# Kernel optimization log

Hardware: AMD Instinct MI355X
Metric: run time of the kernel (lower is better)

Reference implementation:

```python
import jax, jax.numpy as jnp
import numpy as np

D_MODEL = 1024
NHEAD = 16


def unitnorm(v):
    # F.normalize(v, dim=-1): v / max(||v||_2, 1e-12)
    n = jnp.sqrt(jnp.sum(v * v, axis=-1, keepdims=True))
    return v / jnp.maximum(n, 1e-12)


def setup_inputs() -> dict:
    key = jax.random.key(0)
    ks = jax.random.split(key, 14)
    d = D_MODEL
    sc = 1.0 / np.sqrt(d)
    inp = jax.random.normal(ks[0], (2048, 8, d), dtype=jnp.float32)
    def lin(kw, kb, out_dim):
        W = jax.random.uniform(kw, (out_dim, d), minval=-sc, maxval=sc, dtype=jnp.float32)
        b = jax.random.uniform(kb, (out_dim,), minval=-sc, maxval=sc, dtype=jnp.float32)
        return W, b
    Wq_w, Wq_b = lin(ks[1], ks[2], d)
    Wk_w, Wk_b = lin(ks[3], ks[4], d)
    Wv_w, Wv_b = lin(ks[5], ks[6], d)
    Wo_w, Wo_b = lin(ks[7], ks[8], d)
    Ww_w, Ww_b = lin(ks[9], ks[10], NHEAD)
    Wr_w, Wr_b = lin(ks[11], ks[12], NHEAD)
    return {"inp": inp, "Wq_w": Wq_w, "Wq_b": Wq_b, "Wk_w": Wk_w, "Wk_b": Wk_b,
            "Wv_w": Wv_w, "Wv_b": Wv_b, "Wo_w": Wo_w, "Wo_b": Wo_b,
            "Ww_w": Ww_w, "Ww_b": Ww_b, "Wr_w": Wr_w, "Wr_b": Wr_b}


def reference(inp, Wq_w, Wq_b, Wk_w, Wk_b, Wv_w, Wv_b, Wo_w, Wo_b, Ww_w, Ww_b, Wr_w, Wr_b):
    src = inp  # src=None path
    S, B, d = inp.shape
    n = NHEAD
    # torch Linear: x @ W.T + b
    k = (src @ Wk_w.T + Wk_b).reshape(S, B, n, -1)
    v = (src @ Wv_w.T + Wv_b).reshape(S, B, n, -1)
    q = (inp @ Wq_w.T + Wq_b).reshape(S, B, n, -1)
    k = unitnorm(k)
    q = unitnorm(q)
    w = jax.nn.sigmoid(src @ Ww_w.T + Ww_b)            # [S,B,n]
    A = jnp.einsum('sbnq,sbnv->bnvq', k, v * w[:, :, :, None])
    r = jax.nn.sigmoid(inp @ Wr_w.T + Wr_b)            # [S,B,n]
    out = jnp.einsum('sbnq,bnvq->sbnv', q, A) * r[:, :, :, None]
    out = out.reshape(S, B, d)
    out = out @ Wo_w.T + Wo_b
    return (out, A)
```

## Files before the change

### kernel.cpp

```cpp
#include <hip/hip_runtime.h>
#include <cstdint>
#include <cstddef>


typedef __bf16 bf16x8 __attribute__((ext_vector_type(8)));
typedef float  f32x4  __attribute__((ext_vector_type(4)));
typedef unsigned short u16x8 __attribute__((ext_vector_type(8)));
typedef unsigned short u16x4 __attribute__((ext_vector_type(4)));

#define ROWS 16384
#define DM   1024

__device__ __forceinline__ unsigned short f2bf(float f) {
  unsigned int u = __builtin_bit_cast(unsigned int, f);
  u += 0x7FFFu + ((u >> 16) & 1u);
  return (unsigned short)(u >> 16);
}
__device__ __forceinline__ float bf2f(unsigned short h) {
  unsigned int u = ((unsigned int)h) << 16;
  return __builtin_bit_cast(float, u);
}
__device__ __forceinline__ float sigm(float x) { return 1.0f / (1.0f + __expf(-x)); }

__device__ __forceinline__ void gload_lds16(const void* g, void* l) {
  __builtin_amdgcn_global_load_lds((__attribute__((address_space(1))) void*)(g),
                                   (__attribute__((address_space(3))) void*)(l),
                                   16, 0, 0);
}

__global__ __launch_bounds__(256) void k_cast_x(const float* __restrict__ X,
                                                unsigned short* __restrict__ Xb) {
  size_t i = ((size_t)blockIdx.x * 256 + threadIdx.x) * 8;
  f32x4 a = *(const f32x4*)(X + i);
  f32x4 b = *(const f32x4*)(X + i + 4);
  u16x8 o;
  o[0] = f2bf(a[0]); o[1] = f2bf(a[1]); o[2] = f2bf(a[2]); o[3] = f2bf(a[3]);
  o[4] = f2bf(b[0]); o[5] = f2bf(b[1]); o[6] = f2bf(b[2]); o[7] = f2bf(b[3]);
  *(u16x8*)(Xb + i) = o;
}

__global__ __launch_bounds__(256) void k_pack_w(
    const float* __restrict__ Wq, const float* __restrict__ Wk, const float* __restrict__ Wv,
    const float* __restrict__ Wo, const float* __restrict__ Ww, const float* __restrict__ Wr,
    const float* __restrict__ bq, const float* __restrict__ bk, const float* __restrict__ bv,
    const float* __restrict__ bw, const float* __restrict__ br,
    unsigned short* __restrict__ Wpack, float* __restrict__ biasP,
    unsigned short* __restrict__ WRw, float* __restrict__ biasWR,
    unsigned short* __restrict__ Wob) {
  int r = blockIdx.x, t = threadIdx.x;
  const float* src; float bias = 0.0f; unsigned short* dst; float* bdst;
  if (r < 1024)      { src = Wq + (size_t)r * DM;          bias = bq[r];        dst = Wpack + (size_t)r * DM;          bdst = biasP + r; }
  else if (r < 2048) { src = Wk + (size_t)(r - 1024) * DM; bias = bk[r - 1024]; dst = Wpack + (size_t)r * DM;          bdst = biasP + r; }
  else if (r < 3072) { src = Wv + (size_t)(r - 2048) * DM; bias = bv[r - 2048]; dst = Wpack + (size_t)r * DM;          bdst = biasP + r; }
  else if (r < 3088) { src = Ww + (size_t)(r - 3072) * DM; bias = bw[r - 3072]; dst = WRw + (size_t)(r - 3072) * DM;   bdst = biasWR + (r - 3072); }
  else if (r < 3104) { src = Wr + (size_t)(r - 3088) * DM; bias = br[r - 3088]; dst = WRw + (size_t)(r - 3072) * DM;   bdst = biasWR + (r - 3072); }
  else               { src = Wo + (size_t)(r - 3104) * DM;                      dst = Wob + (size_t)(r - 3104) * DM;   bdst = nullptr; }
  int c = t * 4;
  f32x4 v = *(const f32x4*)(src + c);
  u16x4 o;
  o[0] = f2bf(v[0]); o[1] = f2bf(v[1]); o[2] = f2bf(v[2]); o[3] = f2bf(v[3]);
  *(u16x4*)(dst + c) = o;
  if (t == 0 && bdst) *bdst = bias;
}

__global__ __launch_bounds__(256) void k_wr(const unsigned short* __restrict__ Xb,
                                            const unsigned short* __restrict__ WRw,
                                            const float* __restrict__ biasWR,
                                            float* __restrict__ WRf) {
  __shared__ __bf16 sA[128 * 64];
  __shared__ __bf16 sB[32 * 64];
  int t = threadIdx.x, lane = t & 63, wid = t >> 6;
  int m0 = blockIdx.x * 128;
  int l15 = lane & 15, l4 = lane >> 4;
  f32x4 acc[2][2];
#pragma unroll
  for (int i = 0; i < 2; ++i)
#pragma unroll
    for (int j = 0; j < 2; ++j) acc[i][j] = (f32x4){0.f, 0.f, 0.f, 0.f};
  int srow = t >> 3, schunk = (t & 7) * 8;
  for (int kt = 0; kt < DM; kt += 64) {
#pragma unroll
    for (int c = 0; c < 4; ++c)
      gload_lds16(Xb + (size_t)(m0 + c * 32 + srow) * DM + kt + schunk,
                  (void*)(sA + c * 2048 + wid * 512));
    gload_lds16(WRw + (size_t)srow * DM + kt + schunk, (void*)(sB + wid * 512));
    __syncthreads();
#pragma unroll
    for (int ks = 0; ks < 2; ++ks) {
      bf16x8 fa[2], fb[2];
#pragma unroll
      for (int mi = 0; mi < 2; ++mi)
        fa[mi] = *(const bf16x8*)(sA + (wid * 32 + mi * 16 + l15) * 64 + (ks * 4 + l4) * 8);
#pragma unroll
      for (int ni = 0; ni < 2; ++ni)
        fb[ni] = *(const bf16x8*)(sB + (ni * 16 + l15) * 64 + (ks * 4 + l4) * 8);
#pragma unroll
      for (int mi = 0; mi < 2; ++mi)
#pragma unroll
        for (int ni = 0; ni < 2; ++ni)
          acc[mi][ni] = __builtin_amdgcn_mfma_f32_16x16x32_bf16(fa[mi], fb[ni], acc[mi][ni], 0, 0, 0);
    }
    __syncthreads();
  }
#pragma unroll
  for (int mi = 0; mi < 2; ++mi)
#pragma unroll
    for (int e = 0; e < 4; ++e) {
      int row = m0 + wid * 32 + mi * 16 + 4 * l4 + e;
#pragma unroll
      for (int ni = 0; ni < 2; ++ni)
        WRf[(size_t)row * 32 + ni * 16 + l15] = acc[mi][ni][e] + biasWR[ni * 16 + l15];
    }
}


#define VMW(N)  asm volatile("s_waitcnt vmcnt(" #N ")" ::: "memory")
#define LGKM(N) asm volatile("s_waitcnt lgkmcnt(" #N ")" ::: "memory")
#define SB0     __builtin_amdgcn_sched_barrier(0)

__device__ __forceinline__ void stageT(const unsigned short* __restrict__ Asrc,
                                       const unsigned short* __restrict__ Bsrc,
                                       int kt, __bf16* sm, int sb, int w) {
#pragma unroll
  for (int c = 0; c < 2; ++c)
    gload_lds16(Asrc + (size_t)c * 128 * DM + kt, (void*)(sm + sb + c * 4096 + w * 512));
#pragma unroll
  for (int c = 0; c < 2; ++c)
    gload_lds16(Bsrc + (size_t)c * 128 * DM + kt, (void*)(sm + sb + 8192 + c * 4096 + w * 512));
}

__device__ __forceinline__ void rdFA(bf16x8 (&fa)[8], const __bf16* base, const int (&aoff)[8]) {
#pragma unroll
  for (int mi = 0; mi < 8; ++mi) fa[mi] = *(const bf16x8*)(base + aoff[mi]);
}
__device__ __forceinline__ void rdFB(bf16x8 (&fb)[4], const __bf16* base, const int (&boff)[4]) {
#pragma unroll
  for (int ni = 0; ni < 4; ++ni) fb[ni] = *(const bf16x8*)(base + boff[ni]);
}

#define MFMA32(FB)                                                                   \
  do {                                                                               \
    __builtin_amdgcn_s_setprio(1);                                                   \
    _Pragma("unroll") for (int mi = 0; mi < 8; ++mi)                                 \
    _Pragma("unroll") for (int ni = 0; ni < 4; ++ni)                                 \
      acc[mi][ni] = __builtin_amdgcn_mfma_f32_16x16x32_bf16(fa[mi], FB[ni],          \
                                                            acc[mi][ni], 0, 0, 0);  \
    __builtin_amdgcn_s_setprio(0);                                                   \
    SB0;                                                                             \
  } while (0)

__device__ __forceinline__ void gemm_d4(const unsigned short* __restrict__ Ag,
                                        const unsigned short* __restrict__ Bg,
                                        __bf16* sm, f32x4 (&acc)[8][4],
                                        int m0, int n0, int lane, int w) {
  const int wm = w >> 2, wn = w & 3;
  const int l15 = lane & 15, l4 = lane >> 4;
  const int t = w * 64 + lane;
  const int srow = t >> 2;
  const int schunk = ((t & 3) ^ ((srow >> 1) & 3)) * 8;
  const unsigned short* Asrc = Ag + (size_t)(m0 + srow) * DM + schunk;
  const unsigned short* Bsrc = Bg + (size_t)(n0 + srow) * DM + schunk;

  int aoff[8], boff[4];
#pragma unroll
  for (int mi = 0; mi < 8; ++mi) {
    int r = wm * 128 + mi * 16 + l15;
    aoff[mi] = r * 32 + ((l4 ^ ((r >> 1) & 3)) << 3);
  }
#pragma unroll
  for (int ni = 0; ni < 4; ++ni) {
    int r = wn * 64 + ni * 16 + l15;
    boff[ni] = 8192 + r * 32 + ((l4 ^ ((r >> 1) & 3)) << 3);
  }

  bf16x8 fa[8], fbA[4], fbB[4];
  stageT(Asrc, Bsrc, 0,  sm, 0,     w);
  stageT(Asrc, Bsrc, 32, sm, 16384, w);
  stageT(Asrc, Bsrc, 64, sm, 32768, w);
  VMW(8);
  __builtin_amdgcn_s_barrier(); SB0;
  rdFB(fbA, sm, boff);
  rdFA(fa, sm, aoff);
  VMW(4);
  __builtin_amdgcn_s_barrier(); SB0;

  int sb = 49152;
  int rb = 16384;
  for (int i = 0; i < 14; ++i) {
    stageT(Asrc, Bsrc, (2 * i + 3) * 32, sm, sb, w); sb = (sb + 16384) & 65535;
    rdFB(fbB, sm + rb, boff);
    LGKM(4); SB0;
    MFMA32(fbA);
    rdFA(fa, sm + rb, aoff); rb = (rb + 16384) & 65535;
    VMW(4);
    __builtin_amdgcn_s_barrier(); SB0;
    stageT(Asrc, Bsrc, (2 * i + 4) * 32, sm, sb, w); sb = (sb + 16384) & 65535;
    rdFB(fbA, sm + rb, boff);
    LGKM(4); SB0;
    MFMA32(fbB);
    rdFA(fa, sm + rb, aoff); rb = (rb + 16384) & 65535;
    VMW(4);
    __builtin_amdgcn_s_barrier(); SB0;
  }
  stageT(Asrc, Bsrc, 992, sm, sb, w);
  rdFB(fbB, sm + rb, boff);
  LGKM(4); SB0;
  MFMA32(fbA);
  rdFA(fa, sm + rb, aoff); rb = (rb + 16384) & 65535;
  VMW(4);
  __builtin_amdgcn_s_barrier(); SB0;
  rdFB(fbA, sm + rb, boff);
  LGKM(4); SB0;
  MFMA32(fbB);
  rdFA(fa, sm + rb, aoff); rb = (rb + 16384) & 65535;
  VMW(0);
  __builtin_amdgcn_s_barrier(); SB0;
  rdFB(fbB, sm + rb, boff);
  LGKM(4); SB0;
  MFMA32(fbA);
  rdFA(fa, sm + rb, aoff);
  LGKM(0); SB0;
  MFMA32(fbB);
}

__global__ __launch_bounds__(512, 2) void k_gemm_qkv6(
    const unsigned short* __restrict__ Xb, const unsigned short* __restrict__ Wpack,
    const float* __restrict__ biasP, const float* __restrict__ WRf,
    unsigned short* __restrict__ Qb, unsigned short* __restrict__ Kb,
    unsigned short* __restrict__ Vb) {
  __shared__ __bf16 sm[65536];
  const int t = threadIdx.x, lane = t & 63, w = t >> 6;
  const int wm = w >> 2, wn = w & 3;
  const int l15 = lane & 15, l4 = lane >> 4;
  int orig = blockIdx.x;
  int wg = (orig & 7) * 96 + (orig >> 3);
  const int m0 = (wg & 63) << 8;
  const int n0 = (wg >> 6) << 8;
  f32x4 acc[8][4];
#pragma unroll
  for (int i = 0; i < 8; ++i)
#pragma unroll
    for (int j = 0; j < 4; ++j) acc[i][j] = (f32x4){0.f, 0.f, 0.f, 0.f};
  gemm_d4(Xb, Wpack, sm, acc, m0, n0, lane, w);

  const int colbase = n0 + wn * 64;
  float bb[4];
#pragma unroll
  for (int ni = 0; ni < 4; ++ni) bb[ni] = biasP[colbase + ni * 16 + l15];

  if (colbase < 2048) {
    unsigned short* dstp = (colbase < 1024) ? Qb : Kb;
    int coff = (colbase < 1024) ? colbase : (colbase - 1024);
#pragma unroll
    for (int mi = 0; mi < 8; ++mi)
#pragma unroll
      for (int e = 0; e < 4; ++e) {
        float v[4]; float ssq = 0.f;
#pragma unroll
        for (int ni = 0; ni < 4; ++ni) { v[ni] = acc[mi][ni][e] + bb[ni]; ssq += v[ni] * v[ni]; }
        ssq += __shfl_xor(ssq, 1);
        ssq += __shfl_xor(ssq, 2);
        ssq += __shfl_xor(ssq, 4);
        ssq += __shfl_xor(ssq, 8);
        float sc = 1.0f / fmaxf(sqrtf(ssq), 1e-12f);
        int row = m0 + wm * 128 + mi * 16 + 4 * l4 + e;
#pragma unroll
        for (int ni = 0; ni < 4; ++ni)
          dstp[(size_t)row * DM + coff + ni * 16 + l15] = f2bf(v[ni] * sc);
      }
  } else {
    int hv = (colbase - 2048) >> 6;
    int coff = colbase - 2048;
#pragma unroll
    for (int mi = 0; mi < 8; ++mi)
#pragma unroll
      for (int e = 0; e < 4; ++e) {
        int row = m0 + wm * 128 + mi * 16 + 4 * l4 + e;
        float wgt = sigm(WRf[(size_t)row * 32 + hv]);
#pragma unroll
        for (int ni = 0; ni < 4; ++ni)
          Vb[(size_t)row * DM + coff + ni * 16 + l15] = f2bf((acc[mi][ni][e] + bb[ni]) * wgt);
      }
  }
}

__global__ __launch_bounds__(512, 2) void k_gemm_out6(
    const unsigned short* __restrict__ Ob, const unsigned short* __restrict__ Wob,
    const float* __restrict__ bo, float* __restrict__ Out) {
  __shared__ __bf16 sm[65536];
  const int t = threadIdx.x, lane = t & 63, w = t >> 6;
  const int wm = w >> 2, wn = w & 3;
  const int l15 = lane & 15, l4 = lane >> 4;
  int orig = blockIdx.x;
  int wg = (orig & 7) * 32 + (orig >> 3);
  const int m0 = (wg & 63) << 8;
  const int n0 = (wg >> 6) << 8;
  f32x4 acc[8][4];
#pragma unroll
  for (int i = 0; i < 8; ++i)
#pragma unroll
    for (int j = 0; j < 4; ++j) acc[i][j] = (f32x4){0.f, 0.f, 0.f, 0.f};
  gemm_d4(Ob, Wob, sm, acc, m0, n0, lane, w);

  float bb[4];
#pragma unroll
  for (int ni = 0; ni < 4; ++ni) bb[ni] = bo[n0 + wn * 64 + ni * 16 + l15];
#pragma unroll
  for (int mi = 0; mi < 8; ++mi)
#pragma unroll
    for (int e = 0; e < 4; ++e) {
      int row = m0 + wm * 128 + mi * 16 + 4 * l4 + e;
#pragma unroll
      for (int ni = 0; ni < 4; ++ni) {
        int col = n0 + wn * 64 + ni * 16 + l15;
        Out[(size_t)row * DM + col] = acc[mi][ni][e] + bb[ni];
      }
    }
}

__global__ __launch_bounds__(256, 2) void k_gemm_A(const unsigned short* __restrict__ Kb,
                                                   const unsigned short* __restrict__ Vb,
                                                   float* __restrict__ Apart) {
  __shared__ __bf16 sK[64 * 64];
  __shared__ __bf16 sV[64 * 64];
  int t = threadIdx.x, lane = t & 63, wid = t >> 6;
  int bn = blockIdx.x & 127, sk = blockIdx.x >> 7;
  int b = bn >> 4, n = bn & 15;
  f32x4 acc[4];
#pragma unroll
  for (int j = 0; j < 4; j++) acc[j] = (f32x4){0.f, 0.f, 0.f, 0.f};
  int lrow = lane >> 3, lcol = (lane & 7) * 8;

  for (int st = sk * 1024; st < (sk + 1) * 1024; st += 64) {
#pragma unroll
    for (int c = 0; c < 2; c++) {
      int r0 = wid * 16 + c * 8;
      size_t g = ((size_t)(st + r0 + lrow) * 8 + b) * DM + n * 64 + lcol;
      gload_lds16(Kb + g, (void*)(sK + r0 * 64));
      gload_lds16(Vb + g, (void*)(sV + r0 * 64));
    }
    __syncthreads();
#pragma unroll
    for (int kk = 0; kk < 64; kk += 32) {
      bf16x8 av, bv[4];
#pragma unroll
      for (int e = 0; e < 8; e++)
        av[e] = sV[(kk + 8 * (lane >> 4) + e) * 64 + wid * 16 + (lane & 15)];
#pragma unroll
      for (int jn = 0; jn < 4; jn++)
#pragma unroll
        for (int e = 0; e < 8; e++)
          bv[jn][e] = sK[(kk + 8 * (lane >> 4) + e) * 64 + jn * 16 + (lane & 15)];
#pragma unroll
      for (int jn = 0; jn < 4; jn++)
        acc[jn] = __builtin_amdgcn_mfma_f32_16x16x32_bf16(av, bv[jn], acc[jn], 0, 0, 0);
    }
    __syncthreads();
  }
  float* Ap = Apart + (size_t)(sk * 128 + bn) * 4096;
#pragma unroll
  for (int jn = 0; jn < 4; jn++) {
#pragma unroll
    for (int e = 0; e < 4; e++) {
      int i = wid * 16 + 4 * (lane >> 4) + e;
      int j = jn * 16 + (lane & 15);
      Ap[i * 64 + j] = acc[jn][e];
    }
  }
}

__global__ __launch_bounds__(256) void k_reduceA(const float* __restrict__ Apart,
                                                 float* __restrict__ Aout,
                                                 unsigned short* __restrict__ Abf) {
  int bn = blockIdx.x, t = threadIdx.x;
  size_t base = (size_t)bn * 4096 + t * 16;
#pragma unroll
  for (int j = 0; j < 4; ++j) {
    f32x4 x = *(const f32x4*)(Apart + base + j * 4);
    f32x4 y = *(const f32x4*)(Apart + (size_t)128 * 4096 + base + j * 4);
    x += y;
    *(f32x4*)(Aout + base + j * 4) = x;
    u16x4 o;
    o[0] = f2bf(x[0]); o[1] = f2bf(x[1]); o[2] = f2bf(x[2]); o[3] = f2bf(x[3]);
    *(u16x4*)(Abf + base + j * 4) = o;
  }
}

__global__ __launch_bounds__(256, 2) void k_gemm_o2(const unsigned short* __restrict__ Qb,
                                                    const unsigned short* __restrict__ Abf,
                                                    const float* __restrict__ WRf,
                                                    unsigned short* __restrict__ Ob) {
  __shared__ __bf16 sQ[128 * 64];
  __shared__ __bf16 sA[64 * 64];
  int t = threadIdx.x, lane = t & 63, wid = t >> 6;
  int bn = blockIdx.x & 127, stile = blockIdx.x >> 7;
  int b = bn >> 4, n = bn & 15;
  int s0 = stile * 128;
  int lrow = lane >> 3, lcol = (lane & 7) * 8;
#pragma unroll
  for (int c = 0; c < 4; c++) {
    int r0 = wid * 32 + c * 8;
    gload_lds16(Qb + ((size_t)(s0 + r0 + lrow) * 8 + b) * DM + n * 64 + lcol,
                (void*)(sQ + r0 * 64));
  }
#pragma unroll
  for (int c = 0; c < 2; c++) {
    int r0 = wid * 16 + c * 8;
    gload_lds16(Abf + (size_t)bn * 4096 + (size_t)(r0 + lrow) * 64 + lcol,
                (void*)(sA + r0 * 64));
  }
  __syncthreads();
  f32x4 acc[2][4];
#pragma unroll
  for (int i = 0; i < 2; i++)
#pragma unroll
    for (int j = 0; j < 4; j++) acc[i][j] = (f32x4){0.f, 0.f, 0.f, 0.f};
#pragma unroll
  for (int kk = 0; kk < 64; kk += 32) {
    bf16x8 aq[2], bA[4];
#pragma unroll
    for (int mi = 0; mi < 2; mi++)
      aq[mi] = *(const bf16x8*)(sQ + (wid * 32 + mi * 16 + (lane & 15)) * 64 + kk + 8 * (lane >> 4));
#pragma unroll
    for (int ni = 0; ni < 4; ni++)
      bA[ni] = *(const bf16x8*)(sA + (ni * 16 + (lane & 15)) * 64 + kk + 8 * (lane >> 4));
#pragma unroll
    for (int mi = 0; mi < 2; mi++)
#pragma unroll
      for (int ni = 0; ni < 4; ni++)
        acc[mi][ni] = __builtin_amdgcn_mfma_f32_16x16x32_bf16(aq[mi], bA[ni], acc[mi][ni], 0, 0, 0);
  }
#pragma unroll
  for (int mi = 0; mi < 2; mi++) {
#pragma unroll
    for (int e = 0; e < 4; e++) {
      int srow = wid * 32 + mi * 16 + 4 * (lane >> 4) + e;
      size_t row = (size_t)(s0 + srow) * 8 + b;
      float rv = sigm(WRf[row * 32 + 16 + n]);
#pragma unroll
      for (int ni = 0; ni < 4; ni++)
        Ob[row * DM + n * 64 + ni * 16 + (lane & 15)] = f2bf(acc[mi][ni][e] * rv);
    }
  }
}

extern "C" void kernel_launch(void* const* d_in, const int* in_sizes, int n_in,
                              void* d_out, int out_size, void* d_ws, size_t ws_size,
                              hipStream_t stream) {
  (void)in_sizes; (void)n_in; (void)out_size; (void)ws_size;
  const float* X  = (const float*)d_in[0];
  const float* Wq = (const float*)d_in[1];  const float* bq = (const float*)d_in[2];
  const float* Wk = (const float*)d_in[3];  const float* bk = (const float*)d_in[4];
  const float* Wv = (const float*)d_in[5];  const float* bv = (const float*)d_in[6];
  const float* Wo = (const float*)d_in[7];  const float* bo = (const float*)d_in[8];
  const float* Ww = (const float*)d_in[9];  const float* bw = (const float*)d_in[10];
  const float* Wr = (const float*)d_in[11]; const float* br = (const float*)d_in[12];

  char* ws = (char*)d_ws;
  unsigned short* Wpack = (unsigned short*)(ws + 0);
  float*          Apart = (float*)(ws + 0);
  unsigned short* Abf   = (unsigned short*)(ws + 4194304);
  float*          biasP = (float*)(ws + 6291456);
  unsigned short* WRw   = (unsigned short*)(ws + 6303744);
  float*          biasWR= (float*)(ws + 6369280);
  unsigned short* Wob   = (unsigned short*)(ws + 6369408);
  unsigned short* Xb    = (unsigned short*)(ws + 8466560);
  unsigned short* Ob    = Xb;
  unsigned short* Qb    = (unsigned short*)(ws + 42020992);
  unsigned short* Kb    = (unsigned short*)(ws + 75575424);
  unsigned short* Vb    = (unsigned short*)(ws + 109129856);
  float*          WRf   = (float*)(ws + 142684288);

  float* Out0 = (float*)d_out;
  float* Aout = Out0 + (size_t)ROWS * DM;

  k_cast_x<<<dim3(8192), dim3(256), 0, stream>>>(X, Xb);
  k_pack_w<<<dim3(4128), dim3(256), 0, stream>>>(Wq, Wk, Wv, Wo, Ww, Wr,
                                                 bq, bk, bv, bw, br,
                                                 Wpack, biasP, WRw, biasWR, Wob);
  k_wr<<<dim3(128), dim3(256), 0, stream>>>(Xb, WRw, biasWR, WRf);
  k_gemm_qkv6<<<dim3(768), dim3(512), 0, stream>>>(Xb, Wpack, biasP, WRf, Qb, Kb, Vb);
  k_gemm_A<<<dim3(256), dim3(256), 0, stream>>>(Kb, Vb, Apart);
  k_reduceA<<<dim3(128), dim3(256), 0, stream>>>(Apart, Aout, Abf);
  k_gemm_o2<<<dim3(2048), dim3(256), 0, stream>>>(Qb, Abf, WRf, Ob);
  k_gemm_out6<<<dim3(256), dim3(512), 0, stream>>>(Ob, Wob, bo, Out0);
}
```

Baseline: 241.9 us.

## Replace QKV GEMM with 128x128-tile double-buffered kernel at higher occupancy

The fused QKV projection GEMM moves from a 256x256-tile, 512-thread, hand-pipelined kernel to a simpler 128x128-tile, 256-thread kernel with two LDS buffers and 3 blocks per CU, launched as 3072 blocks. The aim is more blocks per CU and a less rigid schedule to hide latency, and the normalize and sigmoid epilogues are kept the same. The cost is lower data reuse per tile, so global and LDS traffic rise, and the hand-tuned waitcnt/barrier pipelining is gone. The output GEMM is only renamed.

Measured after the change: 256.8 us. +6.2%, slower.

```diff
diff --git a/kernel.cpp b/kernel.cpp
--- a/kernel.cpp
+++ b/kernel.cpp
@@ -114,6 +114,121 @@
 }
 
 
+#define STAGE128(P, kt)                                                             \
+  do {                                                                              \
+    _Pragma("unroll") for (int c = 0; c < 2; ++c)                                   \
+      gload_lds16(Asrc + (size_t)(c * 64) * DM + (kt),                              \
+                  (void*)(sm + (P) * 8192 + c * 2048 + w * 512));                   \
+    _Pragma("unroll") for (int c = 0; c < 2; ++c)                                   \
+      gload_lds16(Bsrc + (size_t)(c * 64) * DM + (kt),                              \
+                  (void*)(sm + (P) * 8192 + 4096 + c * 2048 + w * 512));            \
+  } while (0)
+
+__device__ __forceinline__ void gemm128(const unsigned short* __restrict__ Ag,
+                                        const unsigned short* __restrict__ Bg,
+                                        __bf16* sm, f32x4 (&acc)[4][4],
+                                        int m0, int n0, int lane, int w) {
+  const int wr = w >> 1, wc = w & 1;
+  const int l15 = lane & 15, l4 = lane >> 4;
+  const int t = w * 64 + lane;
+  const int srow = t >> 2;
+  const int sc = ((t & 3) ^ ((srow >> 1) & 3)) * 8;
+  const unsigned short* Asrc = Ag + (size_t)(m0 + srow) * DM + sc;
+  const unsigned short* Bsrc = Bg + (size_t)(n0 + srow) * DM + sc;
+
+  int aoff[4], boff[4];
+#pragma unroll
+  for (int mi = 0; mi < 4; ++mi) {
+    int r = wr * 64 + mi * 16 + l15;
+    aoff[mi] = r * 32 + ((l4 ^ ((r >> 1) & 3)) << 3);
+  }
+#pragma unroll
+  for (int ni = 0; ni < 4; ++ni) {
+    int r = wc * 64 + ni * 16 + l15;
+    boff[ni] = 4096 + r * 32 + ((l4 ^ ((r >> 1) & 3)) << 3);
+  }
+
+  STAGE128(0, 0);
+  __syncthreads();
+  for (int kt = 0; kt < 32; ++kt) {
+    int P = kt & 1;
+    if (kt < 31) STAGE128(P ^ 1, (kt + 1) * 32);
+    const __bf16* base = sm + P * 8192;
+    bf16x8 fa[4], fb[4];
+#pragma unroll
+    for (int mi = 0; mi < 4; ++mi) fa[mi] = *(const bf16x8*)(base + aoff[mi]);
+#pragma unroll
+    for (int ni = 0; ni < 4; ++ni) fb[ni] = *(const bf16x8*)(base + boff[ni]);
+#pragma unroll
+    for (int mi = 0; mi < 4; ++mi)
+#pragma unroll
+      for (int ni = 0; ni < 4; ++ni)
+        acc[mi][ni] = __builtin_amdgcn_mfma_f32_16x16x32_bf16(fa[mi], fb[ni], acc[mi][ni], 0, 0, 0);
+    __syncthreads();
+  }
+}
+
+__global__ __launch_bounds__(256, 3) void k_gemm_qkv9(
+    const unsigned short* __restrict__ Xb, const unsigned short* __restrict__ Wpack,
+    const float* __restrict__ biasP, const float* __restrict__ WRf,
+    unsigned short* __restrict__ Qb, unsigned short* __restrict__ Kb,
+    unsigned short* __restrict__ Vb) {
+  __shared__ __bf16 sm[16384];
+  const int t = threadIdx.x, lane = t & 63, w = t >> 6;
+  const int wr = w >> 1, wc = w & 1;
+  const int l15 = lane & 15, l4 = lane >> 4;
+  int orig = blockIdx.x;
+  int wg = (orig & 7) * 384 + (orig >> 3);
+  const int m0 = (wg / 24) << 7;
+  const int n0 = (wg % 24) << 7;
+  f32x4 acc[4][4];
+#pragma unroll
+  for (int i = 0; i < 4; ++i)
+#pragma unroll
+    for (int j = 0; j < 4; ++j) acc[i][j] = (f32x4){0.f, 0.f, 0.f, 0.f};
+  gemm128(Xb, Wpack, sm, acc, m0, n0, lane, w);
+
+  const int colbase = n0 + wc * 64;
+  float bb[4];
+#pragma unroll
+  for (int ni = 0; ni < 4; ++ni) bb[ni] = biasP[colbase + ni * 16 + l15];
+
+  if (colbase < 2048) {
+    unsigned short* dstp = (colbase < 1024) ? Qb : Kb;
+    int coff = (colbase < 1024) ? colbase : (colbase - 1024);
+#pragma unroll
+    for (int mi = 0; mi < 4; ++mi)
+#pragma unroll
+      for (int e = 0; e < 4; ++e) {
+        float v[4]; float ssq = 0.f;
+#pragma unroll
+        for (int ni = 0; ni < 4; ++ni) { v[ni] = acc[mi][ni][e] + bb[ni]; ssq += v[ni] * v[ni]; }
+        ssq += __shfl_xor(ssq, 1);
+        ssq += __shfl_xor(ssq, 2);
+        ssq += __shfl_xor(ssq, 4);
+        ssq += __shfl_xor(ssq, 8);
+        float sc2 = 1.0f / fmaxf(sqrtf(ssq), 1e-12f);
+        int row = m0 + wr * 64 + mi * 16 + 4 * l4 + e;
+#pragma unroll
+        for (int ni = 0; ni < 4; ++ni)
+          dstp[(size_t)row * DM + coff + ni * 16 + l15] = f2bf(v[ni] * sc2);
+      }
+  } else {
+    int hv = (colbase - 2048) >> 6;
+    int coff = colbase - 2048;
+#pragma unroll
+    for (int mi = 0; mi < 4; ++mi)
+#pragma unroll
+      for (int e = 0; e < 4; ++e) {
+        int row = m0 + wr * 64 + mi * 16 + 4 * l4 + e;
+        float wgt = sigm(WRf[(size_t)row * 32 + hv]);
+#pragma unroll
+        for (int ni = 0; ni < 4; ++ni)
+          Vb[(size_t)row * DM + coff + ni * 16 + l15] = f2bf((acc[mi][ni][e] + bb[ni]) * wgt);
+      }
+  }
+}
+
 #define VMW(N)  asm volatile("s_waitcnt vmcnt(" #N ")" ::: "memory")
 #define LGKM(N) asm volatile("s_waitcnt lgkmcnt(" #N ")" ::: "memory")
 #define SB0     __builtin_amdgcn_sched_barrier(0)
@@ -223,68 +338,7 @@
   MFMA32(fbB);
 }
 
-__global__ __launch_bounds__(512, 2) void k_gemm_qkv6(
-    const unsigned short* __restrict__ Xb, const unsigned short* __restrict__ Wpack,
-    const float* __restrict__ biasP, const float* __restrict__ WRf,
-    unsigned short* __restrict__ Qb, unsigned short* __restrict__ Kb,
-    unsigned short* __restrict__ Vb) {
-  __shared__ __bf16 sm[65536];
-  const int t = threadIdx.x, lane = t & 63, w = t >> 6;
-  const int wm = w >> 2, wn = w & 3;
-  const int l15 = lane & 15, l4 = lane >> 4;
-  int orig = blockIdx.x;
-  int wg = (orig & 7) * 96 + (orig >> 3);
-  const int m0 = (wg & 63) << 8;
-  const int n0 = (wg >> 6) << 8;
-  f32x4 acc[8][4];
-#pragma unroll
-  for (int i = 0; i < 8; ++i)
-#pragma unroll
-    for (int j = 0; j < 4; ++j) acc[i][j] = (f32x4){0.f, 0.f, 0.f, 0.f};
-  gemm_d4(Xb, Wpack, sm, acc, m0, n0, lane, w);
-
-  const int colbase = n0 + wn * 64;
-  float bb[4];
-#pragma unroll
-  for (int ni = 0; ni < 4; ++ni) bb[ni] = biasP[colbase + ni * 16 + l15];
-
-  if (colbase < 2048) {
-    unsigned short* dstp = (colbase < 1024) ? Qb : Kb;
-    int coff = (colbase < 1024) ? colbase : (colbase - 1024);
-#pragma unroll
-    for (int mi = 0; mi < 8; ++mi)
-#pragma unroll
-      for (int e = 0; e < 4; ++e) {
-        float v[4]; float ssq = 0.f;
-#pragma unroll
-        for (int ni = 0; ni < 4; ++ni) { v[ni] = acc[mi][ni][e] + bb[ni]; ssq += v[ni] * v[ni]; }
-        ssq += __shfl_xor(ssq, 1);
-        ssq += __shfl_xor(ssq, 2);
-        ssq += __shfl_xor(ssq, 4);
-        ssq += __shfl_xor(ssq, 8);
-        float sc = 1.0f / fmaxf(sqrtf(ssq), 1e-12f);
-        int row = m0 + wm * 128 + mi * 16 + 4 * l4 + e;
-#pragma unroll
-        for (int ni = 0; ni < 4; ++ni)
-          dstp[(size_t)row * DM + coff + ni * 16 + l15] = f2bf(v[ni] * sc);
-      }
-  } else {
-    int hv = (colbase - 2048) >> 6;
-    int coff = colbase - 2048;
-#pragma unroll
-    for (int mi = 0; mi < 8; ++mi)
-#pragma unroll
-      for (int e = 0; e < 4; ++e) {
-        int row = m0 + wm * 128 + mi * 16 + 4 * l4 + e;
-        float wgt = sigm(WRf[(size_t)row * 32 + hv]);
-#pragma unroll
-        for (int ni = 0; ni < 4; ++ni)
-          Vb[(size_t)row * DM + coff + ni * 16 + l15] = f2bf((acc[mi][ni][e] + bb[ni]) * wgt);
-      }
-  }
-}
-
-__global__ __launch_bounds__(512, 2) void k_gemm_out6(
+__global__ __launch_bounds__(512, 2) void k_gemm_out9(
     const unsigned short* __restrict__ Ob, const unsigned short* __restrict__ Wob,
     const float* __restrict__ bo, float* __restrict__ Out) {
   __shared__ __bf16 sm[65536];
@@ -479,9 +533,9 @@
                                                  bq, bk, bv, bw, br,
                                                  Wpack, biasP, WRw, biasWR, Wob);
   k_wr<<<dim3(128), dim3(256), 0, stream>>>(Xb, WRw, biasWR, WRf);
-  k_gemm_qkv6<<<dim3(768), dim3(512), 0, stream>>>(Xb, Wpack, biasP, WRf, Qb, Kb, Vb);
+  k_gemm_qkv9<<<dim3(3072), dim3(256), 0, stream>>>(Xb, Wpack, biasP, WRf, Qb, Kb, Vb);
   k_gemm_A<<<dim3(256), dim3(256), 0, stream>>>(Kb, Vb, Apart);
   k_reduceA<<<dim3(128), dim3(256), 0, stream>>>(Apart, Aout, Abf);
   k_gemm_o2<<<dim3(2048), dim3(256), 0, stream>>>(Qb, Abf, WRf, Ob);
-  k_gemm_out6<<<dim3(256), dim3(512), 0, stream>>>(Ob, Wob, bo, Out0);
-}
+  k_gemm_out9<<<dim3(256), dim3(512), 0, stream>>>(Ob, Wob, bo, Out0);
+}
```
